# Optimization experiments

Hardware: AMD Instinct MI355X
Metric: run time of the kernel (lower is better)

The kernel has to match this reference:

```python
import jax, jax.numpy as jnp
import numpy as np

NU, NT, E, H = 100000, 200000, 1000000, 64
NUM_LAYERS = 3


def setup_inputs() -> dict:
    key = jax.random.key(0)
    ks = jax.random.split(key, 16)
    s = 0.05
    inp = {}
    inp["x_user"] = jax.random.normal(ks[0], (NU, 32), jnp.float32)
    inp["x_transaction"] = jax.random.normal(ks[1], (NT, 64), jnp.float32)
    inp["ei_u2u"] = jax.random.randint(ks[2], (2, E), 0, NU, jnp.int32)
    inp["ei_t2t"] = jax.random.randint(ks[3], (2, E), 0, NT, jnp.int32)
    inp["ei_u2t"] = jnp.stack([jax.random.randint(ks[4], (E,), 0, NU),
                               jax.random.randint(ks[5], (E,), 0, NT)]).astype(jnp.int32)
    inp["ei_t2u"] = jnp.stack([jax.random.randint(ks[6], (E,), 0, NT),
                               jax.random.randint(ks[7], (E,), 0, NU)]).astype(jnp.int32)
    inp["W_emb_user"] = jax.random.normal(ks[8], (32, H), jnp.float32) * s
    inp["b_emb_user"] = jnp.zeros((H,), jnp.float32)
    inp["W_emb_txn"] = jax.random.normal(ks[9], (64, H), jnp.float32) * s
    inp["b_emb_txn"] = jnp.zeros((H,), jnp.float32)
    # one GCNConv weight/bias per (layer, edge_type): order u2u, t2t, u2t, t2u
    inp["conv_W"] = jax.random.normal(ks[10], (NUM_LAYERS, 4, H, H), jnp.float32) * s
    inp["conv_b"] = jnp.zeros((NUM_LAYERS, 4, H), jnp.float32)
    inp["W1"] = jax.random.normal(ks[11], (H, H), jnp.float32) * s
    inp["b1"] = jnp.zeros((H,), jnp.float32)
    inp["W2"] = jax.random.normal(ks[12], (H, 1), jnp.float32) * s
    inp["b2"] = jnp.zeros((1,), jnp.float32)
    return inp


def _gcn(h_src, ei, n_src, n_dst, W, b, self_loops):
    """GCNConv: x W with symmetric degree normalization, scatter-sum into dst."""
    src, dst = ei[0], ei[1]
    if self_loops:  # same node type on both ends: add self loops (PyG default)
        loop = jnp.arange(n_dst, dtype=src.dtype)
        src = jnp.concatenate([src, loop])
        dst = jnp.concatenate([dst, loop])
        deg = jax.ops.segment_sum(jnp.ones_like(dst, jnp.float32), dst, num_segments=n_dst)
        dinv = jnp.where(deg > 0, jax.lax.rsqrt(jnp.maximum(deg, 1.0)), 0.0)
        norm = dinv[src] * dinv[dst]
    else:  # bipartite relation: out-degree of src, in-degree of dst
        ds = jax.ops.segment_sum(jnp.ones_like(src, jnp.float32), src, num_segments=n_src)
        dd = jax.ops.segment_sum(jnp.ones_like(dst, jnp.float32), dst, num_segments=n_dst)
        dsi = jnp.where(ds > 0, jax.lax.rsqrt(jnp.maximum(ds, 1.0)), 0.0)
        ddi = jnp.where(dd > 0, jax.lax.rsqrt(jnp.maximum(dd, 1.0)), 0.0)
        norm = dsi[src] * ddi[dst]
    m = h_src @ W  # [N_src, H] transform first (GCNConv order)
    out = jax.ops.segment_sum(m[src] * norm[:, None], dst, num_segments=n_dst)
    return out + b


def reference(x_user, x_transaction, ei_u2u, ei_t2t, ei_u2t, ei_t2u,
              W_emb_user, b_emb_user, W_emb_txn, b_emb_txn,
              conv_W, conv_b, W1, b1, W2, b2):
    hu = x_user @ W_emb_user + b_emb_user          # [NU, H]
    ht = x_transaction @ W_emb_txn + b_emb_txn     # [NT, H]
    for l in range(NUM_LAYERS):
        ou1 = _gcn(hu, ei_u2u, NU, NU, conv_W[l, 0], conv_b[l, 0], True)
        ot1 = _gcn(ht, ei_t2t, NT, NT, conv_W[l, 1], conv_b[l, 1], True)
        ot2 = _gcn(hu, ei_u2t, NU, NT, conv_W[l, 2], conv_b[l, 2], False)
        ou2 = _gcn(ht, ei_t2u, NT, NU, conv_W[l, 3], conv_b[l, 3], False)
        # HeteroConv aggr='mean' across relations per dst type, then ReLU
        hu = jax.nn.relu((ou1 + ou2) * 0.5)
        ht = jax.nn.relu((ot1 + ot2) * 0.5)
    g = jnp.stack([hu.mean(axis=0), ht.mean(axis=0)])  # [2, H] per-type global mean
    x = g.mean(axis=0, keepdims=True)                  # [1, H]
    x = jax.nn.relu(x @ W1 + b1)                       # dropout is identity at eval
    return jax.nn.sigmoid(x @ W2 + b2)                 # [1, 1]
```

## Files before the change

kernel.cpp:

```cpp
#include <hip/hip_runtime.h>
#include <hip/hip_bf16.h>
#include <hip/hip_fp8.h>

#define NU_ 100000
#define NT_ 200000
#define NE_ 1000000
#define HD  64
#define NL  3

#define OFF0 0
#define OFF1 (NU_)
#define OFF2 (NU_ + NT_)
#define OFF3 (NU_ + 2 * NT_)
#define OFF4 (2 * NU_ + 2 * NT_)
#define OFF5 (3 * NU_ + 2 * NT_)
#define HTOT (3 * NU_ + 3 * NT_)
#define RPT2 (NU_ + NT_)

#define NBU 391
#define NBT 782
#define NBTOT2 (NBU + NBT)

#define PB1  512
#define BKP  2048
#define NBKC 147
#define NBKS 147
#define NBKT (NBKC + NBKS)

#define EMU 512
#define EMT 1024
#define GMU 512
#define GMT 1024
#define GBU 3125
#define GBT 6250

typedef float floatx2 __attribute__((ext_vector_type(2)));
typedef _Float16 f16x8 __attribute__((ext_vector_type(8)));
typedef float f32x4 __attribute__((ext_vector_type(4)));
typedef unsigned short u16x8 __attribute__((ext_vector_type(8)));

__device__ __forceinline__ unsigned char enc_fp8(float v) {
    return (unsigned char)__hip_cvt_float_to_fp8(v, __HIP_SATFINITE, __HIP_E4M3);
}

__device__ __forceinline__ float dec1_fp8(unsigned int u) {
    int e = (u >> 3) & 15;
    int m = u & 7;
    int mant = m | (e ? 8 : 0);
    if (u & 0x80) mant = -mant;
    int ex = (e ? e : 1) - 10;
    return (float)mant * __uint_as_float((unsigned int)(ex + 127) << 23);
}

__device__ __forceinline__ void dec4_fp8(unsigned int u, float* f) {
#if __has_builtin(__builtin_amdgcn_cvt_pk_f32_fp8)
    floatx2 lo = __builtin_amdgcn_cvt_pk_f32_fp8((int)u, false);
    floatx2 hi = __builtin_amdgcn_cvt_pk_f32_fp8((int)u, true);
    f[0] = lo.x; f[1] = lo.y; f[2] = hi.x; f[3] = hi.y;
#else
    f[0] = dec1_fp8(u & 0xff);
    f[1] = dec1_fp8((u >> 8) & 0xff);
    f[2] = dec1_fp8((u >> 16) & 0xff);
    f[3] = dec1_fp8((u >> 24) & 0xff);
#endif
}

__global__ void detect_dtype(const unsigned short* __restrict__ x, int* __restrict__ flag, int n) {
    __shared__ int s_big;
    if (threadIdx.x == 0) s_big = 0;
    __syncthreads();
    int big = 0;
    for (int i = threadIdx.x; i < n; i += blockDim.x) {
        float v = __uint_as_float(((unsigned int)x[i]) << 16);
        if (!(fabsf(v) < 1.0e4f)) big = 1;
    }
    if (big) atomicAdd(&s_big, 1);
    __syncthreads();
    if (threadIdx.x == 0) flag[0] = (s_big > 0) ? 0 : 1;
}

struct Ptr10 { const void* p[10]; };

__global__ void cvt_weights(Ptr10 src, float* __restrict__ dst, float* __restrict__ gsum,
                            const int* __restrict__ flag) {
    const int c[11] = {0, 2048, 2112, 6208, 6272, 55424, 56192, 60288, 60352, 60416, 60417};
    int i = blockIdx.x * blockDim.x + threadIdx.x;
    if (i < 64) gsum[i] = 0.f;
    if (i >= 60417) return;
    int r = 0;
#pragma unroll
    for (int k = 1; k < 10; ++k)
        if (i >= c[k]) r = k;
    int e = i - c[r];
    if (flag[0]) {
        unsigned short u = ((const unsigned short*)src.p[r])[e];
        dst[i] = __uint_as_float(((unsigned int)u) << 16);
    } else {
        dst[i] = ((const float*)src.p[r])[e];
    }
}

__device__ __forceinline__ void p1_dev(int bid, const int* __restrict__ eu2u,
                                       const int* __restrict__ et2t,
                                       const int* __restrict__ eu2t,
                                       const int* __restrict__ et2u,
                                       int* __restrict__ gcnt, int* __restrict__ bofs) {
    __shared__ int cnt[NBKT];
    for (int j = threadIdx.x; j < NBKT; j += 256) cnt[j] = 0;
    __syncthreads();
    for (int i = bid * 256 + threadIdx.x; i < 6 * NE_; i += PB1 * 256) {
        int b;
        if (i < 4 * NE_) {
            int m;
            if (i < NE_)          m = eu2u[i + NE_];
            else if (i < 2 * NE_) m = NU_ + et2t[i];
            else if (i < 3 * NE_) m = NU_ + eu2t[i - NE_];
            else                  m = et2u[i - 2 * NE_];
            b = m >> 11;
        } else {
            int m2 = (i < 5 * NE_) ? eu2t[i - 4 * NE_] : (NU_ + et2u[i - 5 * NE_]);
            b = NBKC + (m2 >> 11);
        }
        atomicAdd(&cnt[b], 1);
    }
    __syncthreads();
    for (int j = threadIdx.x; j < NBKT; j += 256) {
        bofs[bid * NBKT + j] = atomicAdd(&gcnt[j], cnt[j]);
    }
}

template <int K>
__device__ __forceinline__ void embed_mfma_dev(int t0, int tstride, int ntiles,
                                               const void* __restrict__ x,
                                               const float* __restrict__ W,
                                               const float* __restrict__ bias,
                                               _Float16* __restrict__ out,
                                               const int* __restrict__ flag) {
    constexpr int KS = K / 32;
    const int lane = threadIdx.x & 63;
    const int rq = lane & 15;
    const int oct = lane >> 4;

    f16x8 bf[4][KS];
#pragma unroll
    for (int ct = 0; ct < 4; ++ct)
#pragma unroll
        for (int s = 0; s < KS; ++s) {
            const float* wp = W + (size_t)(32 * s + 8 * oct) * HD + 16 * ct + rq;
            f16x8 v;
#pragma unroll
            for (int j = 0; j < 8; ++j) v[j] = (_Float16)wp[(size_t)j * HD];
            bf[ct][s] = v;
        }
    float bv[4];
#pragma unroll
    for (int ct = 0; ct < 4; ++ct) bv[ct] = bias[16 * ct + rq];

    const bool isb = flag[0] != 0;

    for (int t = t0; t < ntiles; t += tstride) {
        const int r0 = t << 4;
        f16x8 a[KS];
        if (isb) {
            const unsigned short* xr = (const unsigned short*)x + (size_t)(r0 + rq) * K + 8 * oct;
#pragma unroll
            for (int s = 0; s < KS; ++s) {
                u16x8 uv = *(const u16x8*)(xr + 32 * s);
                f16x8 v;
#pragma unroll
                for (int j = 0; j < 8; ++j)
                    v[j] = (_Float16)__uint_as_float(((unsigned int)uv[j]) << 16);
                a[s] = v;
            }
        } else {
            const float* xr = (const float*)x + (size_t)(r0 + rq) * K + 8 * oct;
#pragma unroll
            for (int s = 0; s < KS; ++s) {
                float4 x0 = *(const float4*)(xr + 32 * s);
                float4 x1 = *(const float4*)(xr + 32 * s + 4);
                f16x8 v;
                v[0] = (_Float16)x0.x; v[1] = (_Float16)x0.y;
                v[2] = (_Float16)x0.z; v[3] = (_Float16)x0.w;
                v[4] = (_Float16)x1.x; v[5] = (_Float16)x1.y;
                v[6] = (_Float16)x1.z; v[7] = (_Float16)x1.w;
                a[s] = v;
            }
        }

        f32x4 acc[4];
#pragma unroll
        for (int ct = 0; ct < 4; ++ct) acc[ct] = (f32x4){0.f, 0.f, 0.f, 0.f};
#pragma unroll
        for (int ct = 0; ct < 4; ++ct)
#pragma unroll
            for (int s = 0; s < KS; ++s)
                acc[ct] = __builtin_amdgcn_mfma_f32_16x16x32_f16(a[s], bf[ct][s], acc[ct], 0, 0, 0);

        const int rb = r0 + (oct << 2);
#pragma unroll
        for (int ct = 0; ct < 4; ++ct)
#pragma unroll
            for (int g = 0; g < 4; ++g)
                out[(size_t)(rb + g) * HD + 16 * ct + rq] = (_Float16)(acc[ct][g] + bv[ct]);
    }
}

__global__ __launch_bounds__(256) void fused_p1_embed(
    const int* __restrict__ eu2u, const int* __restrict__ et2t,
    const int* __restrict__ eu2t, const int* __restrict__ et2u,
    int* __restrict__ gcnt, int* __restrict__ bofs,
    const void* __restrict__ x_user, const void* __restrict__ x_txn,
    const float* __restrict__ Wembu, const float* __restrict__ bembu,
    const float* __restrict__ Wembt, const float* __restrict__ bembt,
    _Float16* __restrict__ hu, _Float16* __restrict__ ht, const int* __restrict__ flag) {
    int b = blockIdx.x;
    int wid = threadIdx.x >> 6;
    if (b < PB1) {
        p1_dev(b, eu2u, et2t, eu2t, et2u, gcnt, bofs);
    } else if (b < PB1 + EMU) {
        embed_mfma_dev<32>((b - PB1) * 4 + wid, EMU * 4, NU_ / 16, x_user, Wembu, bembu,
                           hu, flag);
    } else {
        embed_mfma_dev<64>((b - PB1 - EMU) * 4 + wid, EMT * 4, NT_ / 16, x_txn, Wembt, bembt,
                           ht, flag);
    }
}

__global__ void scan_buckets(const int* __restrict__ gcnt, int* __restrict__ gbase) {
    __shared__ int sc[NBKT];
    int t = threadIdx.x;
    if (t < NBKT) sc[t] = gcnt[t];
    __syncthreads();
    if (t == 0) {
        int s = 0;
        for (int j = 0; j < NBKC; ++j) { int c = sc[j]; sc[j] = s; s += c; }
        s = 0;
        for (int j = NBKC; j < NBKT; ++j) { int c = sc[j]; sc[j] = s; s += c; }
    }
    __syncthreads();
    if (t < NBKT) gbase[t] = sc[t];
}

__global__ __launch_bounds__(256) void p2_scatter(
    const int* __restrict__ eu2u, const int* __restrict__ et2t,
    const int* __restrict__ eu2t, const int* __restrict__ et2u,
    const int* __restrict__ gbase, const int* __restrict__ bofs,
    uint2* __restrict__ part_csr, unsigned int* __restrict__ part_src) {
    __shared__ int lofs[NBKT];
    for (int j = threadIdx.x; j < NBKT; j += 256) lofs[j] = 0;
    __syncthreads();
    const int bid = blockIdx.x;
    for (int i = bid * 256 + threadIdx.x; i < 6 * NE_; i += PB1 * 256) {
        if (i < 4 * NE_) {
            int m; unsigned int p;
            if (i < NE_)          { m = eu2u[i + NE_];           p = ((unsigned int)eu2u[i]) << 6; }
            else if (i < 2 * NE_) { m = NU_ + et2t[i];           p = ((unsigned int)et2t[i - NE_]) << 6; }
            else if (i < 3 * NE_) { m = NU_ + eu2t[i - NE_];     p = (((unsigned int)eu2t[i - 2 * NE_]) << 6) | 0x80000000u; }
            else                  { m = et2u[i - 2 * NE_];       p = (((unsigned int)et2u[i - 3 * NE_]) << 6) | 0x80000000u; }
            int b = m >> 11;
            int l = atomicAdd(&lofs[b], 1);
            int pos = gbase[b] + bofs[bid * NBKT + b] + l;
            part_csr[pos] = make_uint2((unsigned int)m, p);
        } else {
            int m2 = (i < 5 * NE_) ? eu2t[i - 4 * NE_] : (NU_ + et2u[i - 5 * NE_]);
            int b = NBKC + (m2 >> 11);
            int l = atomicAdd(&lofs[b], 1);
            int pos = gbase[b] + bofs[bid * NBKT + b] + l;
            part_src[pos] = (unsigned int)m2;
        }
    }
}

__global__ __launch_bounds__(1024) void bucket_count(const uint2* __restrict__ part_csr,
                                                     const unsigned int* __restrict__ part_src,
                                                     const int* __restrict__ gcnt,
                                                     const int* __restrict__ gbase,
                                                     int* __restrict__ hist) {
    __shared__ int cA[BKP];
    __shared__ int cB[BKP];
    const int b = blockIdx.x;
    const int n = gcnt[b];
    const int base = gbase[b];
    const int t = threadIdx.x;
    for (int j = t; j < BKP; j += 1024) { cA[j] = 0; cB[j] = 0; }
    __syncthreads();
    if (b < NBKC) {
        for (int i = t; i < n; i += 1024) {
            uint2 it = part_csr[base + i];
            int l = (int)(it.x & (BKP - 1));
            if (it.y >> 31) atomicAdd(&cB[l], 1);
            else            atomicAdd(&cA[l], 1);
        }
        __syncthreads();
        const int m0 = b << 11;
        for (int j = t; j < BKP; j += 1024) {
            int m = m0 + j;
            if (m < NU_ + NT_) {
                int oA = (m < NU_) ? (OFF0 + m) : (OFF1 + (m - NU_));
                int oB = (m < NU_) ? (OFF3 + m) : (OFF2 + (m - NU_));
                hist[oA] = cA[j];
                hist[oB] = cB[j];
            }
        }
    } else {
        for (int i = t; i < n; i += 1024) {
            unsigned int m2 = part_src[base + i];
            atomicAdd(&cA[(int)(m2 & (BKP - 1))], 1);
        }
        __syncthreads();
        const int m0 = (b - NBKC) << 11;
        for (int j = t; j < BKP; j += 1024) {
            int m2 = m0 + j;
            if (m2 < NU_ + NT_) {
                int o = (m2 < NU_) ? (OFF4 + m2) : (OFF5 + (m2 - NU_));
                hist[o] = cA[j];
            }
        }
    }
}

__global__ __launch_bounds__(1024) void bucket_place(const uint2* __restrict__ part_csr,
                                                     const int* __restrict__ gcnt,
                                                     const int* __restrict__ gbase,
                                                     const int* __restrict__ rp,
                                                     int* __restrict__ colU,
                                                     int* __restrict__ colT) {
    __shared__ int fl[BKP];
    const int b = blockIdx.x;
    const int n = gcnt[b];
    const int base = gbase[b];
    const int t = threadIdx.x;
    for (int j = t; j < BKP; j += 1024) fl[j] = 0;
    __syncthreads();
    for (int i = t; i < n; i += 1024) {
        uint2 it = part_csr[base + i];
        int m = (int)it.x;
        int ofs = atomicAdd(&fl[m & (BKP - 1)], 1);
        if (m < NU_) colU[rp[m] + ofs] = (int)it.y;
        else         colT[rp[m] + ofs] = (int)it.y;
    }
}

__device__ __forceinline__ void gemm_mfma_dev(int t0, int tstride, int ntiles,
                                              const _Float16* __restrict__ h,
                                              const float* __restrict__ WA,
                                              const float* __restrict__ WB,
                                              const float* __restrict__ scA,
                                              const float* __restrict__ scB,
                                              unsigned char* __restrict__ mA,
                                              unsigned char* __restrict__ mB) {
    const int lane = threadIdx.x & 63;
    const int rq = lane & 15;
    const int oct = lane >> 4;

    f16x8 bf[2][4][2];
#pragma unroll
    for (int m = 0; m < 2; ++m) {
        const float* W = m ? WB : WA;
#pragma unroll
        for (int ct = 0; ct < 4; ++ct)
#pragma unroll
            for (int s = 0; s < 2; ++s) {
                const float* wp = W + (size_t)(32 * s + 8 * oct) * HD + 16 * ct + rq;
                f16x8 v;
#pragma unroll
                for (int j = 0; j < 8; ++j) v[j] = (_Float16)wp[(size_t)j * HD];
                bf[m][ct][s] = v;
            }
    }

    for (int t = t0; t < ntiles; t += tstride) {
        const int r0 = t << 4;
        const _Float16* hr = h + (size_t)(r0 + rq) * HD + 8 * oct;
        f16x8 a0 = *(const f16x8*)(hr);
        f16x8 a1 = *(const f16x8*)(hr + 32);

        f32x4 acc[2][4];
#pragma unroll
        for (int m = 0; m < 2; ++m)
#pragma unroll
            for (int ct = 0; ct < 4; ++ct) acc[m][ct] = (f32x4){0.f, 0.f, 0.f, 0.f};

#pragma unroll
        for (int m = 0; m < 2; ++m)
#pragma unroll
            for (int ct = 0; ct < 4; ++ct) {
                acc[m][ct] = __builtin_amdgcn_mfma_f32_16x16x32_f16(a0, bf[m][ct][0],
                                                                   acc[m][ct], 0, 0, 0);
                acc[m][ct] = __builtin_amdgcn_mfma_f32_16x16x32_f16(a1, bf[m][ct][1],
                                                                   acc[m][ct], 0, 0, 0);
            }

        const int rb = r0 + (oct << 2);
        float sa[4], sb[4];
#pragma unroll
        for (int g = 0; g < 4; ++g) { sa[g] = scA[rb + g]; sb[g] = scB[rb + g]; }
#pragma unroll
        for (int ct = 0; ct < 4; ++ct)
#pragma unroll
            for (int g = 0; g < 4; ++g) {
                mA[(size_t)(rb + g) * HD + 16 * ct + rq] = enc_fp8(acc[0][ct][g] * sa[g]);
                mB[(size_t)(rb + g) * HD + 16 * ct + rq] = enc_fp8(acc[1][ct][g] * sb[g]);
            }
    }
}

__global__ __launch_bounds__(256) void gemm_dual_both(
    const _Float16* __restrict__ hu, const _Float16* __restrict__ ht,
    const float* __restrict__ W0, const float* __restrict__ Wu2t,
    const float* __restrict__ Wt, const float* __restrict__ Wt2u,
    const float* __restrict__ dinv,
    unsigned char* __restrict__ m_uu, unsigned char* __restrict__ m_ut,
    unsigned char* __restrict__ m_tt, unsigned char* __restrict__ m_tu) {
    int b = blockIdx.x;
    int wid = threadIdx.x >> 6;
    if (b < GMU) {
        gemm_mfma_dev(b * 4 + wid, GMU * 4, NU_ / 16, hu, W0, Wu2t,
                      dinv + OFF0, dinv + OFF4, m_uu, m_ut);
    } else {
        gemm_mfma_dev((b - GMU) * 4 + wid, GMT * 4, NT_ / 16, ht, Wt, Wt2u,
                      dinv + OFF1, dinv + OFF5, m_tt, m_tu);
    }
}

__device__ __forceinline__ void gather_dev(int blk, const unsigned char* __restrict__ msg,
                                           unsigned int offB,
                                           const int4* __restrict__ meta,
                                           const int* __restrict__ col,
                                           const float* __restrict__ ba,
                                           const float* __restrict__ bb,
                                           _Float16* __restrict__ out, int N) {
    const int lane = threadIdx.x & 63;
    const int grp = lane >> 3;
    const int sub = lane & 7;
    const int d = (blk << 5) + ((threadIdx.x >> 6) << 3) + grp;
    const bool valid = d < N;

    int4 mt = make_int4(0, 0, 0, 0);
    if (valid) mt = meta[d];
    const int st = mt.x;
    const int cnt = mt.y;
    const float dA = __int_as_float(mt.z);
    const float dB = __int_as_float(mt.w);
    const unsigned char* msgL = msg + (sub << 3);

    floatx2 acc[4];
#pragma unroll
    for (int q = 0; q < 4; ++q) acc[q] = (floatx2){0.f, 0.f};

    auto consume = [&](uint2 u, float s) {
        floatx2 s2; s2.x = s; s2.y = s;
#if __has_builtin(__builtin_amdgcn_cvt_pk_f32_fp8)
        acc[0] += __builtin_amdgcn_cvt_pk_f32_fp8((int)u.x, false) * s2;
        acc[1] += __builtin_amdgcn_cvt_pk_f32_fp8((int)u.x, true) * s2;
        acc[2] += __builtin_amdgcn_cvt_pk_f32_fp8((int)u.y, false) * s2;
        acc[3] += __builtin_amdgcn_cvt_pk_f32_fp8((int)u.y, true) * s2;
#else
        float f[8];
        dec4_fp8(u.x, f);
        dec4_fp8(u.y, f + 4);
        acc[0].x += f[0] * s; acc[0].y += f[1] * s;
        acc[1].x += f[2] * s; acc[1].y += f[3] * s;
        acc[2].x += f[4] * s; acc[2].y += f[5] * s;
        acc[3].x += f[6] * s; acc[3].y += f[7] * s;
#endif
    };

    if (valid) {
        uint2 uself = *(const uint2*)(msgL + ((unsigned int)d << 6));
        consume(uself, dA);
    }

    int done = 0;
    while (done < cnt) {
        int rem = cnt - done;
        if (rem > 8) rem = 8;
        int cw = (sub < rem) ? col[st + done + sub] : 0;

        uint2 ub0, ub1, ub2, ub3;
        float sc0, sc1, sc2, sc3;

        auto issue = [&](int p, uint2& ub, float& sc) {
            int c = __shfl(cw, (grp << 3) + p);
            unsigned int off = ((unsigned int)c & 0x7fffffffu) + ((c < 0) ? offB : 0u);
            float sv = (c < 0) ? dB : dA;
            sc = (p < rem) ? sv : 0.f;
            ub = *(const uint2*)(msgL + off);
        };

        issue(0, ub0, sc0);
        issue(1, ub1, sc1);
        issue(2, ub2, sc2);
        issue(3, ub3, sc3);

        consume(ub0, sc0);
        issue(4, ub0, sc0);
        consume(ub1, sc1);
        issue(5, ub1, sc1);
        consume(ub2, sc2);
        issue(6, ub2, sc2);
        consume(ub3, sc3);
        issue(7, ub3, sc3);
        consume(ub0, sc0);
        consume(ub1, sc1);
        consume(ub2, sc2);
        consume(ub3, sc3);

        done += 8;
    }

    if (valid) {
        const int col0 = sub << 3;
        float4 a0 = *(const float4*)(ba + col0);
        float4 a1 = *(const float4*)(ba + col0 + 4);
        float4 c0 = *(const float4*)(bb + col0);
        float4 c1 = *(const float4*)(bb + col0 + 4);
        float af[8] = {acc[0].x, acc[0].y, acc[1].x, acc[1].y,
                       acc[2].x, acc[2].y, acc[3].x, acc[3].y};
        float bf[8] = {a0.x + c0.x, a0.y + c0.y, a0.z + c0.z, a0.w + c0.w,
                       a1.x + c1.x, a1.y + c1.y, a1.z + c1.z, a1.w + c1.w};
        f16x8 o;
#pragma unroll
        for (int k = 0; k < 8; ++k)
            o[k] = (_Float16)fmaxf(af[k] + 0.5f * bf[k], 0.f);
        *(f16x8*)(out + ((size_t)d << 6) + col0) = o;
    }
}

__global__ __launch_bounds__(256) void gather_both(
    const unsigned char* __restrict__ msgU, const unsigned char* __restrict__ msgT,
    const int4* __restrict__ meta,
    const int* __restrict__ colU, const int* __restrict__ colT,
    const float* __restrict__ bU0, const float* __restrict__ bU1,
    const float* __restrict__ bT0, const float* __restrict__ bT1,
    _Float16* __restrict__ hu, _Float16* __restrict__ ht) {
    int b = blockIdx.x;
    if (b < GBU) {
        gather_dev(b, msgU, (unsigned int)NU_ * HD, meta, colU, bU0, bU1, hu, NU_);
    } else {
        gather_dev(b - GBU, msgT, (unsigned int)NT_ * HD, meta + NU_, colT, bT0, bT1, ht, NT_);
    }
}

__global__ __launch_bounds__(256) void scan1m(const int* __restrict__ hist, int* __restrict__ rp,
                                              int* __restrict__ bsums, float* __restrict__ dinv) {
    int b = blockIdx.x, t = threadIdx.x;
    int r, lb, n, rpbase, oA, oB;
    if (b < NBU) { r = 0; lb = b;       n = NU_; rpbase = 0;   oA = OFF0; oB = OFF3; }
    else         { r = 1; lb = b - NBU; n = NT_; rpbase = NU_; oA = OFF1; oB = OFF2; }
    int i = lb * 256 + t;
    int hA = (i < n) ? hist[oA + i] : 0;
    int hB = (i < n) ? hist[oB + i] : 0;
    if (i < n) {
        dinv[oA + i] = rsqrtf((float)hA + 1.0f);
        dinv[oB + i] = (hB > 0) ? rsqrtf((float)hB) : 0.f;
    }
    int v = hA + hB;
    __shared__ int s[256];
    s[t] = v;
    __syncthreads();
    for (int off = 1; off < 256; off <<= 1) {
        int x = (t >= off) ? s[t - off] : 0;
        __syncthreads();
        s[t] += x;
        __syncthreads();
    }
    if (i < n) rp[rpbase + i] = s[t] - v;
    if (t == 255) bsums[r * 1024 + lb] = s[255];
}

__global__ __launch_bounds__(1024) void scan2m(int* __restrict__ bsums) {
    int r = blockIdx.x, t = threadIdx.x;
    const int nb = r ? NBT : NBU;
    int v = (t < nb) ? bsums[r * 1024 + t] : 0;
    __shared__ int s[1024];
    s[t] = v;
    __syncthreads();
    for (int off = 1; off < 1024; off <<= 1) {
        int x = (t >= off) ? s[t - off] : 0;
        __syncthreads();
        s[t] += x;
        __syncthreads();
    }
    if (t < nb) bsums[r * 1024 + t] = s[t] - v;
}

__global__ void scan3m(int* __restrict__ rp, const int* __restrict__ bsums,
                       const int* __restrict__ hist, float* __restrict__ dinv,
                       int4* __restrict__ meta) {
    int gid = blockIdx.x * blockDim.x + threadIdx.x;
    if (gid >= RPT2) return;
    int r = (gid < NU_) ? 0 : 1;
    int base = r ? NU_ : 0;
    int lb = (gid - base) >> 8;
    int rpf = rp[gid] + bsums[r * 1024 + lb];
    rp[gid] = rpf;
    int si = r ? (OFF5 + gid - NU_) : (OFF4 + gid);
    int h = hist[si];
    dinv[si] = (h > 0) ? rsqrtf((float)h) : 0.f;
    int oA = r ? (OFF1 + gid - NU_) : (OFF0 + gid);
    int oB = r ? (OFF2 + gid - NU_) : (OFF3 + gid);
    int hA = hist[oA];
    int hB = hist[oB];
    float dA = 0.5f * rsqrtf((float)hA + 1.0f);
    float dB = (hB > 0) ? 0.5f * rsqrtf((float)hB) : 0.f;
    int4 mt;
    mt.x = rpf;
    mt.y = hA + hB;
    mt.z = __float_as_int(dA);
    mt.w = __float_as_int(dB);
    meta[gid] = mt;
}

__global__ __launch_bounds__(256) void colmean_both(const _Float16* __restrict__ hu,
                                                    const _Float16* __restrict__ ht,
                                                    float* __restrict__ gsum) {
    const bool isU = blockIdx.x < 512;
    const _Float16* h = isU ? hu : ht;
    const int n = isU ? NU_ : NT_;
    const float scale = isU ? 0.5f / NU_ : 0.5f / NT_;
    const int blk = isU ? blockIdx.x : blockIdx.x - 512;
    const int lane = threadIdx.x & 63;
    const int w = threadIdx.x >> 6;
    float s = 0.f;
    for (int r = blk * 4 + w; r < n; r += 512 * 4)
        s += (float)h[(size_t)r * HD + lane];
    __shared__ float red[256];
    red[threadIdx.x] = s;
    __syncthreads();
    if (threadIdx.x < 64) {
        float t = red[threadIdx.x] + red[64 + threadIdx.x] + red[128 + threadIdx.x] +
                  red[192 + threadIdx.x];
        atomicAdd(&gsum[lane], t * scale);
    }
}

__global__ void head(const float* __restrict__ g, const float* __restrict__ W1,
                     const float* __restrict__ b1, const float* __restrict__ W2,
                     const float* __restrict__ b2, const int* __restrict__ flag,
                     void* __restrict__ out) {
    const int c = threadIdx.x;
    float x = b1[c];
    for (int k = 0; k < HD; ++k) x = fmaf(g[k], W1[k * HD + c], x);
    x = fmaxf(x, 0.f);
    float t = x * W2[c];
    for (int off = 32; off; off >>= 1) t += __shfl_down(t, off);
    if (c == 0) {
        float z = t + b2[0];
        float s = 1.f / (1.f + expf(-z));
        if (flag[0]) *(__hip_bfloat16*)out = __float2bfloat16(s);
        else *(float*)out = s;
    }
}

extern "C" void kernel_launch(void* const* d_in, const int* in_sizes, int n_in,
                              void* d_out, int out_size, void* d_ws, size_t ws_size,
                              hipStream_t stream) {
    const void* x_user = d_in[0];
    const void* x_txn  = d_in[1];
    const int* ei_u2u = (const int*)d_in[2];
    const int* ei_t2t = (const int*)d_in[3];
    const int* ei_u2t = (const int*)d_in[4];
    const int* ei_t2u = (const int*)d_in[5];

    float* ws = (float*)d_ws;
    _Float16* hu = (_Float16*)ws;
    _Float16* ht = hu + (size_t)NU_ * HD;
    float* dinv = (float*)(ht + (size_t)NT_ * HD);
    float* wts = dinv + HTOT;
    float* gsum = wts + 60432;
    unsigned char* m_uu = (unsigned char*)(gsum + 64);
    unsigned char* m_tu = m_uu + (size_t)NU_ * HD;
    unsigned char* m_tt = m_tu + (size_t)NT_ * HD;
    unsigned char* m_ut = m_tt + (size_t)NT_ * HD;
    int* hist = (int*)(m_ut + (size_t)NU_ * HD);
    int* aux  = hist + HTOT;
    int* rp   = aux + RPT2;
    int* bsums = rp + RPT2;
    int* colU = bsums + 2048;
    int* colT = colU + 2 * NE_;
    int4* meta = (int4*)(colT + 2 * NE_);
    int* dflag = (int*)(meta + RPT2);

    int* gcnt  = aux;
    int* gbase = gcnt + NBKT;
    int* bofs  = gbase + NBKT;

    uint2* part_csr = (uint2*)m_uu;
    unsigned int* part_src = (unsigned int*)colU;

    float* Wembu = wts;
    float* bembu = Wembu + 2048;
    float* Wembt = bembu + 64;
    float* bembt = Wembt + 4096;
    float* convWf = bembt + 64;
    float* convbf = convWf + 49152;
    float* W1f = convbf + 768;
    float* b1f = W1f + 4096;
    float* W2f = b1f + 64;
    float* b2f = W2f + 64;

    hipMemsetAsync(gcnt, 0, (size_t)NBKT * sizeof(int), stream);

    detect_dtype<<<1, 256, 0, stream>>>((const unsigned short*)x_user, dflag, 2048);
    {
        Ptr10 p;
        for (int k = 0; k < 10; ++k) p.p[k] = d_in[6 + k];
        cvt_weights<<<(60417 + 255) / 256, 256, 0, stream>>>(p, wts, gsum, dflag);
    }

    fused_p1_embed<<<PB1 + EMU + EMT, 256, 0, stream>>>(
        ei_u2u, ei_t2t, ei_u2t, ei_t2u, gcnt, bofs,
        x_user, x_txn, Wembu, bembu, Wembt, bembt, hu, ht, dflag);

    scan_buckets<<<1, 512, 0, stream>>>(gcnt, gbase);
    p2_scatter<<<PB1, 256, 0, stream>>>(ei_u2u, ei_t2t, ei_u2t, ei_t2u,
                                        gbase, bofs, part_csr, part_src);
    bucket_count<<<NBKT, 1024, 0, stream>>>(part_csr, part_src, gcnt, gbase, hist);

    scan1m<<<NBTOT2, 256, 0, stream>>>(hist, rp, bsums, dinv);
    scan2m<<<2, 1024, 0, stream>>>(bsums);
    scan3m<<<(RPT2 + 255) / 256, 256, 0, stream>>>(rp, bsums, hist, dinv, meta);

    bucket_place<<<NBKC, 1024, 0, stream>>>(part_csr, gcnt, gbase, rp, colU, colT);

    for (int l = 0; l < NL; ++l) {
        const float* W0   = convWf + ((size_t)l * 4 + 0) * HD * HD;
        const float* Wt   = convWf + ((size_t)l * 4 + 1) * HD * HD;
        const float* Wu2t = convWf + ((size_t)l * 4 + 2) * HD * HD;
        const float* Wt2u = convWf + ((size_t)l * 4 + 3) * HD * HD;
        const float* B0   = convbf + ((size_t)l * 4 + 0) * HD;
        const float* Bt   = convbf + ((size_t)l * 4 + 1) * HD;
        const float* Bu2t = convbf + ((size_t)l * 4 + 2) * HD;
        const float* Bt2u = convbf + ((size_t)l * 4 + 3) * HD;

        gemm_dual_both<<<GMU + GMT, 256, 0, stream>>>(hu, ht, W0, Wu2t, Wt, Wt2u, dinv,
                                                      m_uu, m_ut, m_tt, m_tu);

        gather_both<<<GBU + GBT, 256, 0, stream>>>(m_uu, m_tt,
                                                   meta, colU, colT,
                                                   B0, Bt2u, Bt, Bu2t, hu, ht);
    }

    colmean_both<<<1024, 256, 0, stream>>>(hu, ht, gsum);
    head<<<1, 64, 0, stream>>>(gsum, W1f, b1f, W2f, b2f, dflag, d_out);
}
```

Before: 641.6 us.

## Prepack fp16 MFMA weights, compact partition entries, fold bucket scan, deepen gather prefetch

Adds a pack_weights kernel that lays out all embedding and conv weights once in the fp16 per-lane MFMA fragment order, so the GEMM and embed kernels load each fragment with one vector read instead of eight strided float loads. Partition entries shrink from uint2 to one packed 32-bit word (source, tag, local bucket index), which halves scatter, count and place traffic. The separate scan_buckets launch is folded into every p2_scatter block, which each recompute the prefix. The gather loop now issues all eight neighbour loads up front and prefetches the next column word, trading more live registers for extra memory-level parallelism.

```diff
diff --git a/kernel.cpp b/kernel.cpp
--- a/kernel.cpp
+++ b/kernel.cpp
@@ -26,6 +26,11 @@
 #define NBKC 147
 #define NBKS 147
 #define NBKT (NBKC + NBKS)
+
+#define WPK_EMBU 0
+#define WPK_EMBT 2048
+#define WPK_CONV 6144
+#define WPK_TOT  55296
 
 #define EMU 512
 #define EMT 1024
@@ -98,6 +103,29 @@
     } else {
         dst[i] = ((const float*)src.p[r])[e];
     }
+}
+
+__global__ void pack_weights(const float* __restrict__ wts, _Float16* __restrict__ wpk) {
+    int gid = blockIdx.x * 256 + threadIdx.x;
+    if (gid >= WPK_TOT) return;
+    const float* W;
+    int r, KS;
+    if (gid < WPK_EMBT) { W = wts; r = gid; KS = 1; }
+    else if (gid < WPK_CONV) { W = wts + 2112; r = gid - WPK_EMBT; KS = 2; }
+    else {
+        int mat = (gid - WPK_CONV) >> 12;
+        W = wts + 6272 + mat * 4096;
+        r = (gid - WPK_CONV) & 4095;
+        KS = 2;
+    }
+    int j = r & 7;
+    int lane = (r >> 3) & 63;
+    int f = r >> 9;
+    int ct = f / KS;
+    int s = f - ct * KS;
+    int k = 32 * s + 8 * (lane >> 4) + j;
+    int n = 16 * ct + (lane & 15);
+    wpk[gid] = (_Float16)W[k * 64 + n];
 }
 
 __device__ __forceinline__ void p1_dev(int bid, const int* __restrict__ eu2u,
@@ -132,7 +160,7 @@
 template <int K>
 __device__ __forceinline__ void embed_mfma_dev(int t0, int tstride, int ntiles,
                                                const void* __restrict__ x,
-                                               const float* __restrict__ W,
+                                               const _Float16* __restrict__ Wpk,
                                                const float* __restrict__ bias,
                                                _Float16* __restrict__ out,
                                                const int* __restrict__ flag) {
@@ -145,13 +173,8 @@
 #pragma unroll
     for (int ct = 0; ct < 4; ++ct)
 #pragma unroll
-        for (int s = 0; s < KS; ++s) {
-            const float* wp = W + (size_t)(32 * s + 8 * oct) * HD + 16 * ct + rq;
-            f16x8 v;
-#pragma unroll
-            for (int j = 0; j < 8; ++j) v[j] = (_Float16)wp[(size_t)j * HD];
-            bf[ct][s] = v;
-        }
+        for (int s = 0; s < KS; ++s)
+            bf[ct][s] = *(const f16x8*)(Wpk + (((ct * KS + s) << 9) + (lane << 3)));
     float bv[4];
 #pragma unroll
     for (int ct = 0; ct < 4; ++ct) bv[ct] = bias[16 * ct + rq];
@@ -210,68 +233,64 @@
     const int* __restrict__ eu2t, const int* __restrict__ et2u,
     int* __restrict__ gcnt, int* __restrict__ bofs,
     const void* __restrict__ x_user, const void* __restrict__ x_txn,
-    const float* __restrict__ Wembu, const float* __restrict__ bembu,
-    const float* __restrict__ Wembt, const float* __restrict__ bembt,
+    const _Float16* __restrict__ wpk,
+    const float* __restrict__ bembu, const float* __restrict__ bembt,
     _Float16* __restrict__ hu, _Float16* __restrict__ ht, const int* __restrict__ flag) {
     int b = blockIdx.x;
     int wid = threadIdx.x >> 6;
     if (b < PB1) {
         p1_dev(b, eu2u, et2t, eu2t, et2u, gcnt, bofs);
     } else if (b < PB1 + EMU) {
-        embed_mfma_dev<32>((b - PB1) * 4 + wid, EMU * 4, NU_ / 16, x_user, Wembu, bembu,
-                           hu, flag);
+        embed_mfma_dev<32>((b - PB1) * 4 + wid, EMU * 4, NU_ / 16, x_user,
+                           wpk + WPK_EMBU, bembu, hu, flag);
     } else {
-        embed_mfma_dev<64>((b - PB1 - EMU) * 4 + wid, EMT * 4, NT_ / 16, x_txn, Wembt, bembt,
-                           ht, flag);
-    }
-}
-
-__global__ void scan_buckets(const int* __restrict__ gcnt, int* __restrict__ gbase) {
-    __shared__ int sc[NBKT];
-    int t = threadIdx.x;
-    if (t < NBKT) sc[t] = gcnt[t];
-    __syncthreads();
-    if (t == 0) {
-        int s = 0;
-        for (int j = 0; j < NBKC; ++j) { int c = sc[j]; sc[j] = s; s += c; }
-        s = 0;
-        for (int j = NBKC; j < NBKT; ++j) { int c = sc[j]; sc[j] = s; s += c; }
-    }
-    __syncthreads();
-    if (t < NBKT) gbase[t] = sc[t];
+        embed_mfma_dev<64>((b - PB1 - EMU) * 4 + wid, EMT * 4, NT_ / 16, x_txn,
+                           wpk + WPK_EMBT, bembt, ht, flag);
+    }
 }
 
 __global__ __launch_bounds__(256) void p2_scatter(
     const int* __restrict__ eu2u, const int* __restrict__ et2t,
     const int* __restrict__ eu2t, const int* __restrict__ et2u,
-    const int* __restrict__ gbase, const int* __restrict__ bofs,
-    uint2* __restrict__ part_csr, unsigned int* __restrict__ part_src) {
+    const int* __restrict__ gcnt, int* __restrict__ gbase, const int* __restrict__ bofs,
+    unsigned int* __restrict__ part_csr, unsigned int* __restrict__ part_src) {
+    __shared__ int gb[NBKT];
     __shared__ int lofs[NBKT];
-    for (int j = threadIdx.x; j < NBKT; j += 256) lofs[j] = 0;
+    const int t = threadIdx.x;
+    for (int j = t; j < NBKT; j += 256) { lofs[j] = 0; gb[j] = gcnt[j]; }
+    __syncthreads();
+    if (t == 0) {
+        int s = 0;
+        for (int j = 0; j < NBKC; ++j) { int c = gb[j]; gb[j] = s; s += c; }
+        s = 0;
+        for (int j = NBKC; j < NBKT; ++j) { int c = gb[j]; gb[j] = s; s += c; }
+    }
     __syncthreads();
     const int bid = blockIdx.x;
-    for (int i = bid * 256 + threadIdx.x; i < 6 * NE_; i += PB1 * 256) {
+    if (bid == 0)
+        for (int j = t; j < NBKT; j += 256) gbase[j] = gb[j];
+    for (int i = bid * 256 + t; i < 6 * NE_; i += PB1 * 256) {
         if (i < 4 * NE_) {
-            int m; unsigned int p;
-            if (i < NE_)          { m = eu2u[i + NE_];           p = ((unsigned int)eu2u[i]) << 6; }
-            else if (i < 2 * NE_) { m = NU_ + et2t[i];           p = ((unsigned int)et2t[i - NE_]) << 6; }
-            else if (i < 3 * NE_) { m = NU_ + eu2t[i - NE_];     p = (((unsigned int)eu2t[i - 2 * NE_]) << 6) | 0x80000000u; }
-            else                  { m = et2u[i - 2 * NE_];       p = (((unsigned int)et2u[i - 3 * NE_]) << 6) | 0x80000000u; }
+            int m; unsigned int src, tag;
+            if (i < NE_)          { m = eu2u[i + NE_];        src = (unsigned int)eu2u[i];           tag = 0u; }
+            else if (i < 2 * NE_) { m = NU_ + et2t[i];        src = (unsigned int)et2t[i - NE_];     tag = 1u; tag = 0u; }
+            else if (i < 3 * NE_) { m = NU_ + eu2t[i - NE_];  src = (unsigned int)eu2t[i - 2 * NE_]; tag = 1u; }
+            else                  { m = et2u[i - 2 * NE_];    src = (unsigned int)et2u[i - 3 * NE_]; tag = 1u; }
             int b = m >> 11;
             int l = atomicAdd(&lofs[b], 1);
-            int pos = gbase[b] + bofs[bid * NBKT + b] + l;
-            part_csr[pos] = make_uint2((unsigned int)m, p);
+            int pos = gb[b] + bofs[bid * NBKT + b] + l;
+            part_csr[pos] = (src << 12) | (tag << 11) | (unsigned int)(m & (BKP - 1));
         } else {
             int m2 = (i < 5 * NE_) ? eu2t[i - 4 * NE_] : (NU_ + et2u[i - 5 * NE_]);
             int b = NBKC + (m2 >> 11);
             int l = atomicAdd(&lofs[b], 1);
-            int pos = gbase[b] + bofs[bid * NBKT + b] + l;
+            int pos = gb[b] + bofs[bid * NBKT + b] + l;
             part_src[pos] = (unsigned int)m2;
         }
     }
 }
 
-__global__ __launch_bounds__(1024) void bucket_count(const uint2* __restrict__ part_csr,
+__global__ __launch_bounds__(1024) void bucket_count(const unsigned int* __restrict__ part_csr,
                                                      const unsigned int* __restrict__ part_src,
                                                      const int* __restrict__ gcnt,
                                                      const int* __restrict__ gbase,
@@ -286,10 +305,10 @@
     __syncthreads();
     if (b < NBKC) {
         for (int i = t; i < n; i += 1024) {
-            uint2 it = part_csr[base + i];
-            int l = (int)(it.x & (BKP - 1));
-            if (it.y >> 31) atomicAdd(&cB[l], 1);
-            else            atomicAdd(&cA[l], 1);
+            unsigned int it = part_csr[base + i];
+            int l = (int)(it & (BKP - 1));
+            if (it & 0x800u) atomicAdd(&cB[l], 1);
+            else             atomicAdd(&cA[l], 1);
         }
         __syncthreads();
         const int m0 = b << 11;
@@ -319,7 +338,7 @@
     }
 }
 
-__global__ __launch_bounds__(1024) void bucket_place(const uint2* __restrict__ part_csr,
+__global__ __launch_bounds__(1024) void bucket_place(const unsigned int* __restrict__ part_csr,
                                                      const int* __restrict__ gcnt,
                                                      const int* __restrict__ gbase,
                                                      const int* __restrict__ rp,
@@ -332,19 +351,22 @@
     const int t = threadIdx.x;
     for (int j = t; j < BKP; j += 1024) fl[j] = 0;
     __syncthreads();
+    const int m0 = b << 11;
     for (int i = t; i < n; i += 1024) {
-        uint2 it = part_csr[base + i];
-        int m = (int)it.x;
-        int ofs = atomicAdd(&fl[m & (BKP - 1)], 1);
-        if (m < NU_) colU[rp[m] + ofs] = (int)it.y;
-        else         colT[rp[m] + ofs] = (int)it.y;
+        unsigned int it = part_csr[base + i];
+        int mlow = (int)(it & (BKP - 1));
+        int m = m0 + mlow;
+        int ofs = atomicAdd(&fl[mlow], 1);
+        int colv = (int)(((it >> 12) << 6) | ((it & 0x800u) << 20));
+        if (m < NU_) colU[rp[m] + ofs] = colv;
+        else         colT[rp[m] + ofs] = colv;
     }
 }
 
 __device__ __forceinline__ void gemm_mfma_dev(int t0, int tstride, int ntiles,
                                               const _Float16* __restrict__ h,
-                                              const float* __restrict__ WA,
-                                              const float* __restrict__ WB,
+                                              const _Float16* __restrict__ WApk,
+                                              const _Float16* __restrict__ WBpk,
                                               const float* __restrict__ scA,
                                               const float* __restrict__ scB,
                                               unsigned char* __restrict__ mA,
@@ -356,17 +378,12 @@
     f16x8 bf[2][4][2];
 #pragma unroll
     for (int m = 0; m < 2; ++m) {
-        const float* W = m ? WB : WA;
+        const _Float16* P = m ? WBpk : WApk;
 #pragma unroll
         for (int ct = 0; ct < 4; ++ct)
 #pragma unroll
-            for (int s = 0; s < 2; ++s) {
-                const float* wp = W + (size_t)(32 * s + 8 * oct) * HD + 16 * ct + rq;
-                f16x8 v;
-#pragma unroll
-                for (int j = 0; j < 8; ++j) v[j] = (_Float16)wp[(size_t)j * HD];
-                bf[m][ct][s] = v;
-            }
+            for (int s = 0; s < 2; ++s)
+                bf[m][ct][s] = *(const f16x8*)(P + ((((ct << 1) + s) << 9) + (lane << 3)));
     }
 
     for (int t = t0; t < ntiles; t += tstride) {
@@ -407,8 +424,8 @@
 
 __global__ __launch_bounds__(256) void gemm_dual_both(
     const _Float16* __restrict__ hu, const _Float16* __restrict__ ht,
-    const float* __restrict__ W0, const float* __restrict__ Wu2t,
-    const float* __restrict__ Wt, const float* __restrict__ Wt2u,
+    const _Float16* __restrict__ W0, const _Float16* __restrict__ Wu2t,
+    const _Float16* __restrict__ Wt, const _Float16* __restrict__ Wt2u,
     const float* __restrict__ dinv,
     unsigned char* __restrict__ m_uu, unsigned char* __restrict__ m_ut,
     unsigned char* __restrict__ m_tt, unsigned char* __restrict__ m_tu) {
@@ -471,20 +488,19 @@
         consume(uself, dA);
     }
 
+    int cw = (sub < cnt) ? col[st + sub] : 0;
     int done = 0;
     while (done < cnt) {
         int rem = cnt - done;
         if (rem > 8) rem = 8;
-        int cw = (sub < rem) ? col[st + done + sub] : 0;
-
-        uint2 ub0, ub1, ub2, ub3;
-        float sc0, sc1, sc2, sc3;
+
+        uint2 ub0, ub1, ub2, ub3, ub4, ub5, ub6, ub7;
+        float sc0, sc1, sc2, sc3, sc4, sc5, sc6, sc7;
 
         auto issue = [&](int p, uint2& ub, float& sc) {
             int c = __shfl(cw, (grp << 3) + p);
             unsigned int off = ((unsigned int)c & 0x7fffffffu) + ((c < 0) ? offB : 0u);
-            float sv = (c < 0) ? dB : dA;
-            sc = (p < rem) ? sv : 0.f;
+            sc = (p < rem) ? ((c < 0) ? dB : dA) : 0.f;
             ub = *(const uint2*)(msgL + off);
         };
 
@@ -492,21 +508,25 @@
         issue(1, ub1, sc1);
         issue(2, ub2, sc2);
         issue(3, ub3, sc3);
-
-        consume(ub0, sc0);
-        issue(4, ub0, sc0);
-        consume(ub1, sc1);
-        issue(5, ub1, sc1);
-        consume(ub2, sc2);
-        issue(6, ub2, sc2);
-        consume(ub3, sc3);
-        issue(7, ub3, sc3);
+        issue(4, ub4, sc4);
+        issue(5, ub5, sc5);
+        issue(6, ub6, sc6);
+        issue(7, ub7, sc7);
+
+        int nd = done + 8;
+        int cw2 = (nd + sub < cnt) ? col[st + nd + sub] : 0;
+
         consume(ub0, sc0);
         consume(ub1, sc1);
         consume(ub2, sc2);
         consume(ub3, sc3);
-
-        done += 8;
+        consume(ub4, sc4);
+        consume(ub5, sc5);
+        consume(ub6, sc6);
+        consume(ub7, sc7);
+
+        cw = cw2;
+        done = nd;
     }
 
     if (valid) {
@@ -669,7 +689,8 @@
     float* dinv = (float*)(ht + (size_t)NT_ * HD);
     float* wts = dinv + HTOT;
     float* gsum = wts + 60432;
-    unsigned char* m_uu = (unsigned char*)(gsum + 64);
+    _Float16* wpk = (_Float16*)(gsum + 64);
+    unsigned char* m_uu = (unsigned char*)(wpk + WPK_TOT);
     unsigned char* m_tu = m_uu + (size_t)NU_ * HD;
     unsigned char* m_tt = m_tu + (size_t)NT_ * HD;
     unsigned char* m_ut = m_tt + (size_t)NT_ * HD;
@@ -686,16 +707,13 @@
     int* gbase = gcnt + NBKT;
     int* bofs  = gbase + NBKT;
 
-    uint2* part_csr = (uint2*)m_uu;
+    unsigned int* part_csr = (unsigned int*)m_uu;
     unsigned int* part_src = (unsigned int*)colU;
 
-    float* Wembu = wts;
-    float* bembu = Wembu + 2048;
-    float* Wembt = bembu + 64;
-    float* bembt = Wembt + 4096;
-    float* convWf = bembt + 64;
-    float* convbf = convWf + 49152;
-    float* W1f = convbf + 768;
+    float* bembu = wts + 2048;
+    float* bembt = wts + 6208;
+    float* convbf = wts + 55424;
+    float* W1f = wts + 56192;
     float* b1f = W1f + 4096;
     float* W2f = b1f + 64;
     float* b2f = W2f + 64;
@@ -708,14 +726,14 @@
         for (int k = 0; k < 10; ++k) p.p[k] = d_in[6 + k];
         cvt_weights<<<(60417 + 255) / 256, 256, 0, stream>>>(p, wts, gsum, dflag);
     }
+    pack_weights<<<(WPK_TOT + 255) / 256, 256, 0, stream>>>(wts, wpk);
 
     fused_p1_embed<<<PB1 + EMU + EMT, 256, 0, stream>>>(
         ei_u2u, ei_t2t, ei_u2t, ei_t2u, gcnt, bofs,
-        x_user, x_txn, Wembu, bembu, Wembt, bembt, hu, ht, dflag);
-
-    scan_buckets<<<1, 512, 0, stream>>>(gcnt, gbase);
+        x_user, x_txn, wpk, bembu, bembt, hu, ht, dflag);
+
     p2_scatter<<<PB1, 256, 0, stream>>>(ei_u2u, ei_t2t, ei_u2t, ei_t2u,
-                                        gbase, bofs, part_csr, part_src);
+                                        gcnt, gbase, bofs, part_csr, part_src);
     bucket_count<<<NBKT, 1024, 0, stream>>>(part_csr, part_src, gcnt, gbase, hist);
 
     scan1m<<<NBTOT2, 256, 0, stream>>>(hist, rp, bsums, dinv);
@@ -725,10 +743,10 @@
     bucket_place<<<NBKC, 1024, 0, stream>>>(part_csr, gcnt, gbase, rp, colU, colT);
 
     for (int l = 0; l < NL; ++l) {
-        const float* W0   = convWf + ((size_t)l * 4 + 0) * HD * HD;
-        const float* Wt   = convWf + ((size_t)l * 4 + 1) * HD * HD;
-        const float* Wu2t = convWf + ((size_t)l * 4 + 2) * HD * HD;
-        const float* Wt2u = convWf + ((size_t)l * 4 + 3) * HD * HD;
+        const _Float16* W0   = wpk + WPK_CONV + ((size_t)l * 4 + 0) * 4096;
+        const _Float16* Wt   = wpk + WPK_CONV + ((size_t)l * 4 + 1) * 4096;
+        const _Float16* Wu2t = wpk + WPK_CONV + ((size_t)l * 4 + 2) * 4096;
+        const _Float16* Wt2u = wpk + WPK_CONV + ((size_t)l * 4 + 3) * 4096;
         const float* B0   = convbf + ((size_t)l * 4 + 0) * HD;
         const float* Bt   = convbf + ((size_t)l * 4 + 1) * HD;
         const float* Bu2t = convbf + ((size_t)l * 4 + 2) * HD;
```

Result: faster. 610.4 us (-4.9%).
